# Kernel tuning notes

Measured on AMD Instinct MI355X. Metric: run time of the kernel, lower is better.

The kernel has to match this reference:

```python
import jax, jax.numpy as jnp
import numpy as np

B, T = 64, 500
N_EX, N_SK = 10000, 100
H, K = 128, 32


def setup_inputs() -> dict:
    key = jax.random.key(0)
    ks = jax.random.split(key, 32)
    g = lambda i, shape, s=0.05: (jax.random.normal(ks[i], shape, dtype=jnp.float32) * s)
    inp = {
        's_data': jax.random.randint(ks[0], (B, T), 0, N_SK),
        'a_data': jax.random.randint(ks[1], (B, T), 0, 2),
        'e_data': jax.random.randint(ks[2], (B, T), 0, N_EX),
        'at_data': jax.random.randint(ks[3], (B, T), 0, 100),
        'q_matrix': (jax.random.uniform(ks[4], (N_EX + 1, N_SK + 1)) < 0.05).astype(jnp.float32),
        's_embed_w': g(5, (N_SK + 1, H)),
        'a_embed_w': g(6, (2, H)),
        'e_embed_w': g(7, (N_EX + 1, H)),
        'W1': g(8, (H, 2 * H)), 'b1': jnp.zeros((H,), jnp.float32),
        'W2': g(9, (H, 3 * H)), 'b2': jnp.zeros((H,), jnp.float32),
        'W3': g(10, (H, 2 * H)), 'b3': jnp.zeros((H,), jnp.float32),
        'key_matrix': g(11, (K, H)),
        'gru_w_ih': g(12, (3 * H, H)), 'gru_w_hh': g(13, (3 * H, H)),
        'gru_b_ih': jnp.zeros((3 * H,), jnp.float32), 'gru_b_hh': jnp.zeros((3 * H,), jnp.float32),
        'Wg': g(14, (H, 2 * H)), 'bg': jnp.zeros((H,), jnp.float32),
        'Wgg': g(15, (H, 2 * H)), 'bgg': jnp.zeros((H,), jnp.float32),
        'Wf': g(16, (H, 2 * H)), 'bf': jnp.zeros((H,), jnp.float32),
        'Wp': g(17, (1, 3 * H)), 'bp': jnp.zeros((1,), jnp.float32),
        'Wp1': g(18, (1, 3 * H)), 'bp1': jnp.zeros((1,), jnp.float32),
        'h0': g(19, (H,)),           # xavier init of GRU initial state (shared across batch)
        'm0': g(20, (K, H)),         # xavier init of memory h_pre (shared across batch)
    }
    return inp


def reference(s_data, a_data, e_data, at_data, q_matrix, s_embed_w, a_embed_w, e_embed_w,
              W1, b1, W2, b2, W3, b3, key_matrix, gru_w_ih, gru_w_hh, gru_b_ih, gru_b_hh,
              Wg, bg, Wgg, bgg, Wf, bf, Wp, bp, Wp1, bp1, h0, m0):
    # eval mode: dropout = identity
    Bv, Tv = a_data.shape
    lin = lambda x, W, b: x @ W.T + b
    # ---- embedding (n_exercise > 0 branch) ----
    rel = q_matrix[e_data]                              # [B,T,S+1]
    ssum = rel.sum(-1, keepdims=True)
    ssum = jnp.where(ssum == 0, 1.0, ssum)
    s_emb = jnp.einsum('bts,sh->bth', rel, s_embed_w) / ssum
    e_emb = e_embed_w[e_data]
    a_emb = a_embed_w[a_data]
    se_data = jax.nn.relu(lin(jnp.concatenate([s_emb, e_emb], -1), W1, b1))
    se_learning = jax.nn.relu(lin(jnp.concatenate([s_emb, e_emb, a_emb], -1), W2, b2))
    e_learning = jax.nn.relu(lin(jnp.concatenate([e_emb, a_emb], -1), W3, b3))
    # ---- GRU over e_learning ----
    gx = jnp.einsum('bth,gh->btg', e_learning, gru_w_ih) + gru_b_ih  # [B,T,3H]
    def gru_step(h, gxt):
        gh = h @ gru_w_hh.T + gru_b_hh
        xr, xz, xn = jnp.split(gxt, 3, -1)
        hr, hz, hn = jnp.split(gh, 3, -1)
        r = jax.nn.sigmoid(xr + hr)
        z = jax.nn.sigmoid(xz + hz)
        n = jnp.tanh(xn + r * hn)
        hn2 = (1 - z) * n + z * h
        return hn2, hn2
    _, gru_out = jax.lax.scan(gru_step, jnp.broadcast_to(h0, (Bv, h0.shape[0])), jnp.swapaxes(gx, 0, 1))
    out = jnp.swapaxes(gru_out, 0, 1)[:, :-1]           # [B,T-1,H]
    # ---- key-value memory scan ----
    Wall = jnp.einsum('bth,kh->btk', se_data, key_matrix)  # attention weights (unnormalized)
    h_pre0 = jnp.broadcast_to(m0, (Bv,) + m0.shape)        # [B,K,H]
    ht0 = jnp.einsum('bk,bkh->bh', Wall[:, 0], h_pre0)
    xs = (jnp.swapaxes(Wall[:, :-1], 0, 1),
          jnp.swapaxes(Wall[:, 1:], 0, 1),
          jnp.swapaxes(se_learning[:, :-1], 0, 1))
    def step(carry, x):
        h_pre, ht_pre = carry
        w, w_next, learning = x
        hl = jnp.concatenate([ht_pre, learning], -1)
        gain = jnp.tanh(hl @ Wg.T + bg)
        gate = jax.nn.sigmoid(hl @ Wgg.T + bgg)
        LG = gate * gain                                  # [B,H]
        LG_t = w[:, :, None] * LG[:, None, :]             # [B,K,H] write
        gam = jax.nn.sigmoid(jnp.concatenate([h_pre, jnp.broadcast_to(LG[:, None, :], h_pre.shape)], -1) @ Wf.T + bf)
        h = gam * h_pre + LG_t
        ht = jnp.einsum('bk,bkh->bh', w_next, h)          # read at t+1
        return (h, ht), ht
    _, hts = jax.lax.scan(step, (h_pre0, ht0), xs)
    out1 = jnp.swapaxes(hts, 0, 1)                        # [B,T-1,H]
    sg = jax.lax.stop_gradient
    res = jax.nn.sigmoid(jnp.concatenate([out, sg(out1), e_emb[:, 1:]], -1) @ Wp.T + bp)[..., 0]
    res1 = jax.nn.sigmoid(jnp.concatenate([sg(out), out1, se_data[:, 1:]], -1) @ Wp1.T + bp1)[..., 0]
    pred = jnp.zeros((Bv, Tv), res.dtype).at[:, 1:].set(res * res1)
    return pred
```

## Files before the change

### kernel.cpp

```cpp
#include <hip/hip_runtime.h>

#define TT 500
typedef __attribute__((ext_vector_type(8))) short short8v;
typedef __attribute__((ext_vector_type(4))) short short4v;
typedef __attribute__((ext_vector_type(4))) float float4v;
typedef unsigned short ushort;

__device__ __forceinline__ ushort f2bf(float f) {
  union { float f; unsigned u; } v; v.f = f;
  unsigned r = v.u + 0x7FFFu + ((v.u >> 16) & 1u);
  return (ushort)(r >> 16);
}
__device__ __forceinline__ float bf2f(ushort u) {
  union { unsigned u; float f; } v; v.u = ((unsigned)u) << 16;
  return v.f;
}
__device__ __forceinline__ float sigm(float x) {
  return __builtin_amdgcn_rcpf(1.f + __builtin_amdgcn_exp2f(-1.44269504088896341f * x));
}
__device__ __forceinline__ float tanh_f(float x) {
  return 1.f - 2.f * __builtin_amdgcn_rcpf(1.f + __builtin_amdgcn_exp2f(2.88539008177792682f * x));
}
__device__ __forceinline__ void bar_lds() {
  asm volatile("s_waitcnt lgkmcnt(0)\ns_barrier" ::: "memory");
}
template <int CTRL>
__device__ __forceinline__ float dppadd(float v) {
  int a = __builtin_amdgcn_update_dpp(0, __builtin_bit_cast(int, v), CTRL, 0xF, 0xF, true);
  return v + __builtin_bit_cast(float, a);
}
__device__ __forceinline__ float rsum16(float v) {
  v = dppadd<0xB1>(v);
  v = dppadd<0x4E>(v);
  v = dppadd<0x141>(v);
  v = dppadd<0x140>(v);
  return v;
}
#define MFMA __builtin_amdgcn_mfma_f32_16x16x32_bf16

__global__ __launch_bounds__(256) void conv_k(
    const float* __restrict__ W1, const float* __restrict__ W2,
    const float* __restrict__ W3, const float* __restrict__ Wih,
    const float* __restrict__ key, const float* __restrict__ Wg,
    const float* __restrict__ Wgg, ushort* __restrict__ wts)
{
  int idx = blockIdx.x * 256 + threadIdx.x;
  if (idx >= 200704) return;
  float v;
  if (idx < 32768)       v = W1[idx];
  else if (idx < 81920)  v = W2[idx - 32768];
  else if (idx < 114688) v = W3[idx - 81920];
  else if (idx < 163840) v = Wih[idx - 114688];
  else if (idx < 167936) v = key[idx - 163840];
  else {
    int j = idx - 167936, o = j >> 7, k = j & 127;
    v = (o < 128) ? Wg[o * 256 + 128 + k] : Wgg[(o - 128) * 256 + 128 + k];
  }
  wts[idx] = f2bf(v);
}

#define XS 424
#define SS 648

__global__ __launch_bounds__(256, 2) void phase1_k(
    const int* __restrict__ a_data, const int* __restrict__ e_data,
    const float* __restrict__ qm, const float* __restrict__ semb,
    const float* __restrict__ aemb, const float* __restrict__ eemb,
    const float* __restrict__ b1, const float* __restrict__ b2,
    const float* __restrict__ b3, const float* __restrict__ bih,
    const float* __restrict__ bg, const float* __restrict__ bgg,
    const float* __restrict__ Wp, const float* __restrict__ bp,
    const float* __restrict__ Wp1, const float* __restrict__ bp1,
    const ushort* __restrict__ wts,
    ushort* __restrict__ gxb, ushort* __restrict__ xgx,
    float* __restrict__ wallb, float* __restrict__ c1b, float* __restrict__ c2b)
{
  __shared__ __align__(16) ushort sbuf[27136];
  ushort* Xl = sbuf;
  ushort* Yl = sbuf + 13568;
  ushort* St = sbuf;
  const int tid = threadIdx.x;
  const int b = blockIdx.x >> 4, chunk = blockIdx.x & 15;
  const int t0 = chunk * 32;
  const int NT = (TT - t0 < 32) ? (TT - t0) : 32;
  const ushort* w1b  = wts;
  const ushort* w2b  = wts + 32768;
  const ushort* w3b  = wts + 81920;
  const ushort* wihb = wts + 114688;
  const ushort* keyb = wts + 163840;
  const ushort* wgb  = wts + 167936;

#pragma unroll
  for (int pass = 0; pass < 2; ++pass) {
    const int tok = (tid >> 4) + pass * 16, l16 = tid & 15;
    const int tsrc = (tok < NT) ? tok : (NT - 1);
    const int gt = b * TT + t0 + tsrc;
    const int e = e_data[gt], a = a_data[gt];
    const float* qrow = qm + (size_t)e * 101;
    float qv[7];
#pragma unroll
    for (int i = 0; i < 7; ++i) {
      int s = l16 + 16 * i;
      qv[i] = (s < 101) ? qrow[s] : 0.f;
    }
    const float* sbase = semb + l16 * 8;
    float4v acc0 = {0,0,0,0}, acc1 = {0,0,0,0};
    float cnt = 0.f;
#pragma unroll
    for (int i = 0; i < 7; ++i) {
      unsigned long long bal = __ballot(qv[i] != 0.f);
      unsigned m = (unsigned)((bal >> (tid & 48)) & 0xFFFFull);
      cnt += (float)__popc(m);
      while (m) {
        int s = 16 * i + __builtin_ctz(m);
        m &= m - 1;
        acc0 += *(const float4v*)(sbase + s * 128);
        acc1 += *(const float4v*)(sbase + s * 128 + 4);
      }
    }
    float inv = 1.f / fmaxf(cnt, 1.f);
    ushort* xr = Xl + tok * XS + l16 * 8;
#pragma unroll
    for (int r = 0; r < 4; ++r) { xr[r] = f2bf(acc0[r] * inv); xr[4 + r] = f2bf(acc1[r] * inv); }
    const float* ee = eemb + (size_t)e * 128 + l16 * 8;
    const float* ae = aemb + a * 128 + l16 * 8;
    ushort* xe = Xl + tok * XS + 128 + l16 * 8;
    ushort* xa = Xl + tok * XS + 256 + l16 * 8;
#pragma unroll
    for (int r = 0; r < 8; ++r) { xe[r] = f2bf(ee[r]); xa[r] = f2bf(ae[r]); }
  }
  __syncthreads();

  const int w = tid >> 6, l = tid & 63, jj = l & 15, seg = l >> 4;

  if (tid < 32) {
    int tau = tid;
    if (tau < NT) {
      const ushort* xr = Xl + tau * XS + 128;
      const float* wv = Wp + 256;
      float a0 = bp[0], a1 = 0.f, a2 = 0.f, a3 = 0.f;
      for (int j = 0; j < 128; j += 4) {
        a0 = fmaf(wv[j],     bf2f(xr[j]),     a0);
        a1 = fmaf(wv[j + 1], bf2f(xr[j + 1]), a1);
        a2 = fmaf(wv[j + 2], bf2f(xr[j + 2]), a2);
        a3 = fmaf(wv[j + 3], bf2f(xr[j + 3]), a3);
      }
      c1b[b * TT + t0 + tau] = (a0 + a1) + (a2 + a3);
    }
  }

  short8v axA[12], axB[12];
#pragma unroll
  for (int i = 0; i < 12; ++i) {
    axA[i] = *(short8v*)(Xl + jj * XS + i * 32 + seg * 8);
    axB[i] = *(short8v*)(Xl + (16 + jj) * XS + i * 32 + seg * 8);
  }

  for (int T = w; T < 24; T += 4) {
    float4v dA = {0,0,0,0}, dB = {0,0,0,0};
    float bv;
    if (T < 8) {
      const ushort* Bp = w1b + (T * 16 + jj) * 256 + seg * 8;
      bv = b1[T * 16 + jj];
#pragma unroll
      for (int k = 0; k < 8; ++k) {
        short8v bw = *(const short8v*)(Bp + k * 32);
        dA = MFMA(axA[k], bw, dA, 0, 0, 0);
        dB = MFMA(axB[k], bw, dB, 0, 0, 0);
      }
    } else if (T < 16) {
      const ushort* Bp = w2b + ((T - 8) * 16 + jj) * 384 + seg * 8;
      bv = b2[(T - 8) * 16 + jj];
#pragma unroll
      for (int k = 0; k < 12; ++k) {
        short8v bw = *(const short8v*)(Bp + k * 32);
        dA = MFMA(axA[k], bw, dA, 0, 0, 0);
        dB = MFMA(axB[k], bw, dB, 0, 0, 0);
      }
    } else {
      const ushort* Bp = w3b + ((T - 16) * 16 + jj) * 256 + seg * 8;
      bv = b3[(T - 16) * 16 + jj];
#pragma unroll
      for (int k = 0; k < 8; ++k) {
        short8v bw = *(const short8v*)(Bp + k * 32);
        dA = MFMA(axA[4 + k], bw, dA, 0, 0, 0);
        dB = MFMA(axB[4 + k], bw, dB, 0, 0, 0);
      }
    }
#pragma unroll
    for (int r = 0; r < 4; ++r) {
      float yA = dA[r] + bv, yB = dB[r] + bv;
      Yl[(seg * 4 + r) * XS + T * 16 + jj]        = f2bf(yA > 0.f ? yA : 0.f);
      Yl[(16 + seg * 4 + r) * XS + T * 16 + jj]   = f2bf(yB > 0.f ? yB : 0.f);
    }
  }
  __syncthreads();

  short8v ayA[12], ayB[12];
#pragma unroll
  for (int i = 0; i < 12; ++i) {
    ayA[i] = *(short8v*)(Yl + jj * XS + i * 32 + seg * 8);
    ayB[i] = *(short8v*)(Yl + (16 + jj) * XS + i * 32 + seg * 8);
  }

  if (tid >= 32 && tid < 64) {
    int tau = tid - 32;
    if (tau < NT) {
      const ushort* xr = Yl + tau * XS;
      const float* wv = Wp1 + 256;
      float a0 = bp1[0], a1 = 0.f, a2 = 0.f, a3 = 0.f;
      for (int j = 0; j < 128; j += 4) {
        a0 = fmaf(wv[j],     bf2f(xr[j]),     a0);
        a1 = fmaf(wv[j + 1], bf2f(xr[j + 1]), a1);
        a2 = fmaf(wv[j + 2], bf2f(xr[j + 2]), a2);
        a3 = fmaf(wv[j + 3], bf2f(xr[j + 3]), a3);
      }
      c2b[b * TT + t0 + tau] = (a0 + a1) + (a2 + a3);
    }
  }
  __syncthreads();

  for (int T = w; T < 42; T += 4) {
    const ushort* Bp; int ai;
    if (T < 24)      { Bp = wihb + (T * 16 + jj) * 128 + seg * 8;        ai = 8; }
    else if (T < 40) { Bp = wgb  + ((T - 24) * 16 + jj) * 128 + seg * 8; ai = 4; }
    else             { Bp = keyb + ((T - 40) * 16 + jj) * 128 + seg * 8; ai = 0; }
    float4v dA = {0,0,0,0}, dB = {0,0,0,0};
#pragma unroll
    for (int k = 0; k < 4; ++k) {
      short8v bw = *(const short8v*)(Bp + k * 32);
      dA = MFMA(ayA[ai + k], bw, dA, 0, 0, 0);
      dB = MFMA(ayB[ai + k], bw, dB, 0, 0, 0);
    }
    if (T < 40) {
      float bv = (T < 24) ? bih[T * 16 + jj]
               : (T < 32) ? bg[(T - 24) * 16 + jj] : bgg[(T - 32) * 16 + jj];
      int col = (T < 24) ? (T * 16 + jj) : (384 + (T - 24) * 16 + jj);
#pragma unroll
      for (int r = 0; r < 4; ++r) {
        St[(seg * 4 + r) * SS + col]      = f2bf(dA[r] + bv);
        St[(16 + seg * 4 + r) * SS + col] = f2bf(dB[r] + bv);
      }
    } else {
#pragma unroll
      for (int r = 0; r < 4; ++r) {
        int tokA = seg * 4 + r, tokB = 16 + seg * 4 + r;
        if (tokA < NT)
          wallb[((size_t)(b * TT + t0 + tokA)) * 32 + (T - 40) * 16 + jj] = dA[r];
        if (tokB < NT)
          wallb[((size_t)(b * TT + t0 + tokB)) * 32 + (T - 40) * 16 + jj] = dB[r];
      }
    }
  }
  __syncthreads();

#pragma unroll
  for (int pass = 0; pass < 2; ++pass) {
    const int tok = (tid >> 4) + pass * 16, sg = tid & 15;
    if (tok < NT) {
      size_t gt = (size_t)b * TT + t0 + tok;
#pragma unroll
      for (int p = 0; p < 3; ++p)
        *(short8v*)(gxb + gt * 384 + sg * 24 + p * 8) = *(short8v*)(St + tok * SS + sg * 24 + p * 8);
#pragma unroll
      for (int p = 0; p < 2; ++p)
        *(short8v*)(xgx + gt * 256 + sg * 16 + p * 8) = *(short8v*)(St + tok * SS + 384 + sg * 16 + p * 8);
    }
  }
}

__global__ __launch_bounds__(512) void scan_k(
    const float* __restrict__ Wf, const float* __restrict__ bf_,
    const float* __restrict__ Wg, const float* __restrict__ Wgg,
    const float* __restrict__ Whh, const float* __restrict__ bhh,
    const float* __restrict__ h0v, const float* __restrict__ m0,
    const ushort* __restrict__ gxb, const ushort* __restrict__ xgx,
    const float* __restrict__ wallb,
    ushort* __restrict__ htsm, ushort* __restrict__ htsg)
{
  const int tid = threadIdx.x;
  const int w = tid >> 6, l = tid & 63, jj = l & 15, seg = l >> 4;
  const int n0 = w * 16 + seg * 4;

  if (blockIdx.x < 64) {
    const int b = blockIdx.x;
    __shared__ __align__(16) ushort h_bf[32 * 128];
    __shared__ __align__(16) ushort htb[128];
    __shared__ __align__(16) ushort LGb[128];

    short8v afrA[4], aggA[4], aggB[4], alg[4];
#pragma unroll
    for (int ks = 0; ks < 4; ++ks) {
      const float* sA = Wf  + (w * 16 + jj) * 256 + ks * 32 + seg * 8;
      const float* sB = Wg  + (w * 16 + jj) * 256 + ks * 32 + seg * 8;
      const float* sC = Wgg + (w * 16 + jj) * 256 + ks * 32 + seg * 8;
      const float* sD = Wf  + (w * 16 + jj) * 256 + 128 + ks * 32 + seg * 8;
      short8v a, bb, c, d;
#pragma unroll
      for (int j = 0; j < 8; ++j) {
        a[j] = (short)f2bf(sA[j]); bb[j] = (short)f2bf(sB[j]);
        c[j] = (short)f2bf(sC[j]); d[j] = (short)f2bf(sD[j]);
      }
      afrA[ks] = a; aggA[ks] = bb; aggB[ks] = c; alg[ks] = d;
    }
    const float4v bf4 = *(const float4v*)(bf_ + n0);

    float hreg[2][4];
#pragma unroll
    for (int nt = 0; nt < 2; ++nt) {
      int k = nt * 16 + jj;
      float4v m = *(const float4v*)(m0 + k * 128 + n0);
#pragma unroll
      for (int r = 0; r < 4; ++r) hreg[nt][r] = m[r];
      int p = ((n0 >> 3) + k) & 15;
      short4v pk;
#pragma unroll
      for (int r = 0; r < 4; ++r) pk[r] = (short)f2bf(hreg[nt][r]);
      *(short4v*)(h_bf + k * 128 + p * 8 + (n0 & 7)) = pk;
    }
    const float* wl = wallb + (size_t)b * TT * 32;
    const ushort* xgp = xgx + (size_t)b * TT * 256;
    float wv0 = wl[jj], wv1 = wl[16 + jj];
    float wn0 = wl[32 + jj], wn1 = wl[48 + jj];
    short4v xcg  = *(const short4v*)(xgp + n0);
    short4v xcgg = *(const short4v*)(xgp + 128 + n0);
    short4v xng  = *(const short4v*)(xgp + 256 + n0);
    short4v xngg = *(const short4v*)(xgp + 384 + n0);
    {
      float4v htp;
#pragma unroll
      for (int r = 0; r < 4; ++r)
        htp[r] = rsum16(wv0 * hreg[0][r] + wv1 * hreg[1][r]);
      if (jj == 0) {
        short4v hp;
#pragma unroll
        for (int r = 0; r < 4; ++r) hp[r] = (short)f2bf(htp[r]);
        *(short4v*)(htb + n0) = hp;
      }
    }
    __syncthreads();

    for (int t = 0; t < TT - 1; ++t) {
      int tw = (t + 2 <= TT - 1) ? (t + 2) : (TT - 1);
      float wf0 = wl[tw * 32 + jj], wf1 = wl[tw * 32 + 16 + jj];
      short4v xfg  = *(const short4v*)(xgp + (size_t)tw * 256 + n0);
      short4v xfgg = *(const short4v*)(xgp + (size_t)tw * 256 + 128 + n0);

      short8v hb[4];
#pragma unroll
      for (int ks = 0; ks < 4; ++ks)
        hb[ks] = *(short8v*)(htb + ks * 32 + seg * 8);
      short8v bv0[4], bv1[4];
#pragma unroll
      for (int ks = 0; ks < 4; ++ks) {
        int g = ks * 4 + seg;
        bv0[ks] = *(short8v*)(h_bf + jj * 128 + ((g + jj) & 15) * 8);
        bv1[ks] = *(short8v*)(h_bf + (16 + jj) * 128 + ((g + 16 + jj) & 15) * 8);
      }

      float4v xg4, xgg4;
#pragma unroll
      for (int r = 0; r < 4; ++r) { xg4[r] = bf2f((ushort)xcg[r]); xgg4[r] = bf2f((ushort)xcgg[r]); }
      float4v dg0 = xg4, dg1 = {0,0,0,0}, gg0 = xgg4, gg1 = {0,0,0,0};
      dg0 = MFMA(aggA[0], hb[0], dg0, 0, 0, 0);
      dg0 = MFMA(aggA[1], hb[1], dg0, 0, 0, 0);
      dg1 = MFMA(aggA[2], hb[2], dg1, 0, 0, 0);
      dg1 = MFMA(aggA[3], hb[3], dg1, 0, 0, 0);
      gg0 = MFMA(aggB[0], hb[0], gg0, 0, 0, 0);
      gg0 = MFMA(aggB[1], hb[1], gg0, 0, 0, 0);
      gg1 = MFMA(aggB[2], hb[2], gg1, 0, 0, 0);
      gg1 = MFMA(aggB[3], hb[3], gg1, 0, 0, 0);

      float4v a0A = {0,0,0,0}, a0B = {0,0,0,0}, a1A = {0,0,0,0}, a1B = {0,0,0,0};
      a0A = MFMA(afrA[0], bv0[0], a0A, 0, 0, 0);
      a0A = MFMA(afrA[1], bv0[1], a0A, 0, 0, 0);
      a0B = MFMA(afrA[2], bv0[2], a0B, 0, 0, 0);
      a0B = MFMA(afrA[3], bv0[3], a0B, 0, 0, 0);
      a1A = MFMA(afrA[0], bv1[0], a1A, 0, 0, 0);
      a1A = MFMA(afrA[1], bv1[1], a1A, 0, 0, 0);
      a1B = MFMA(afrA[2], bv1[2], a1B, 0, 0, 0);
      a1B = MFMA(afrA[3], bv1[3], a1B, 0, 0, 0);

      float lgv[4];
#pragma unroll
      for (int r = 0; r < 4; ++r)
        lgv[r] = tanh_f(dg0[r] + dg1[r]) * sigm(gg0[r] + gg1[r]);
      if (jj == 0) {
        short4v lp;
#pragma unroll
        for (int r = 0; r < 4; ++r) lp[r] = (short)f2bf(lgv[r]);
        *(short4v*)(LGb + n0) = lp;
      }
      bar_lds();

      short8v lb[4];
#pragma unroll
      for (int ks = 0; ks < 4; ++ks)
        lb[ks] = *(short8v*)(LGb + ks * 32 + seg * 8);
      float4v dl0 = bf4, dl1 = {0,0,0,0};
      dl0 = MFMA(alg[0], lb[0], dl0, 0, 0, 0);
      dl0 = MFMA(alg[1], lb[1], dl0, 0, 0, 0);
      dl1 = MFMA(alg[2], lb[2], dl1, 0, 0, 0);
      dl1 = MFMA(alg[3], lb[3], dl1, 0, 0, 0);

      float4v htp = {0,0,0,0};
#pragma unroll
      for (int nt = 0; nt < 2; ++nt) {
        float wvv = nt ? wv1 : wv0;
        float wnn = nt ? wn1 : wn0;
#pragma unroll
        for (int r = 0; r < 4; ++r) {
          float a = nt ? (a1A[r] + a1B[r]) : (a0A[r] + a0B[r]);
          float gam = sigm(a + dl0[r] + dl1[r]);
          float hn = fmaf(gam, hreg[nt][r], wvv * lgv[r]);
          hreg[nt][r] = hn;
          htp[r] = fmaf(wnn, hn, htp[r]);
        }
        int k = nt * 16 + jj;
        int p = ((n0 >> 3) + k) & 15;
        short4v pk;
#pragma unroll
        for (int r = 0; r < 4; ++r) pk[r] = (short)f2bf(hreg[nt][r]);
        *(short4v*)(h_bf + k * 128 + p * 8 + (n0 & 7)) = pk;
      }
#pragma unroll
      for (int r = 0; r < 4; ++r) htp[r] = rsum16(htp[r]);
      if (jj == 0) {
        short4v hp;
#pragma unroll
        for (int r = 0; r < 4; ++r) hp[r] = (short)f2bf(htp[r]);
        *(short4v*)(htb + n0) = hp;
        *(short4v*)(htsm + ((size_t)b * TT + t) * 128 + n0) = hp;
      }
      wv0 = wn0; wv1 = wn1; wn0 = wf0; wn1 = wf1;
      xcg = xng; xcgg = xngg; xng = xfg; xngg = xfgg;
      bar_lds();
    }
  } else {
    const int b = blockIdx.x - 64;
    __shared__ __align__(16) ushort hb2[2][128];

    short8v wfr[3][4];
    float4v bfr[3];
#pragma unroll
    for (int i = 0; i < 3; ++i) {
      int Mt = w + i * 8;
#pragma unroll
      for (int ks = 0; ks < 4; ++ks) {
        const float* src = Whh + (Mt * 16 + jj) * 128 + ks * 32 + seg * 8;
        short8v tv;
#pragma unroll
        for (int j = 0; j < 8; ++j) tv[j] = (short)f2bf(src[j]);
        wfr[i][ks] = tv;
      }
      bfr[i] = *(const float4v*)(bhh + Mt * 16 + seg * 4);
    }
    const ushort* gpb = gxb + (size_t)b * TT * 384;
    float4v hj4 = *(const float4v*)(h0v + n0);
    if (jj == 0) {
      short4v hp;
#pragma unroll
      for (int r = 0; r < 4; ++r) hp[r] = (short)f2bf(hj4[r]);
      *(short4v*)(&hb2[0][n0]) = hp;
    }
    short4v xr_c = *(const short4v*)(gpb + n0);
    short4v xz_c = *(const short4v*)(gpb + 128 + n0);
    short4v xn_c = *(const short4v*)(gpb + 256 + n0);
    short4v xr_n = *(const short4v*)(gpb + 384 + n0);
    short4v xz_n = *(const short4v*)(gpb + 512 + n0);
    short4v xn_n = *(const short4v*)(gpb + 640 + n0);
    __syncthreads();

    for (int t = 0; t < TT - 1; ++t) {
      int tf = (t + 2 < TT - 1) ? (t + 2) : (TT - 2);
      const ushort* gf = gpb + (size_t)tf * 384;
      short4v xr_f = *(const short4v*)(gf + n0);
      short4v xz_f = *(const short4v*)(gf + 128 + n0);
      short4v xn_f = *(const short4v*)(gf + 256 + n0);

      const ushort* hsrc = hb2[t & 1];
      short8v bfrg[4];
#pragma unroll
      for (int ks = 0; ks < 4; ++ks)
        bfrg[ks] = *(short8v*)(hsrc + ks * 32 + seg * 8);

      float4v a0A = bfr[0], a1A = bfr[1], a2A = bfr[2];
      float4v a0B = {0,0,0,0}, a1B = {0,0,0,0}, a2B = {0,0,0,0};
      a0A = MFMA(wfr[0][0], bfrg[0], a0A, 0, 0, 0);
      a0A = MFMA(wfr[0][1], bfrg[1], a0A, 0, 0, 0);
      a0B = MFMA(wfr[0][2], bfrg[2], a0B, 0, 0, 0);
      a0B = MFMA(wfr[0][3], bfrg[3], a0B, 0, 0, 0);
      a1A = MFMA(wfr[1][0], bfrg[0], a1A, 0, 0, 0);
      a1A = MFMA(wfr[1][1], bfrg[1], a1A, 0, 0, 0);
      a1B = MFMA(wfr[1][2], bfrg[2], a1B, 0, 0, 0);
      a1B = MFMA(wfr[1][3], bfrg[3], a1B, 0, 0, 0);
      a2A = MFMA(wfr[2][0], bfrg[0], a2A, 0, 0, 0);
      a2A = MFMA(wfr[2][1], bfrg[1], a2A, 0, 0, 0);
      a2B = MFMA(wfr[2][2], bfrg[2], a2B, 0, 0, 0);
      a2B = MFMA(wfr[2][3], bfrg[3], a2B, 0, 0, 0);

      ushort* hdst = (ushort*)hb2[(t + 1) & 1];
      short4v hp;
#pragma unroll
      for (int r = 0; r < 4; ++r) {
        float rr = sigm(bf2f((ushort)xr_c[r]) + a0A[r] + a0B[r]);
        float zz = sigm(bf2f((ushort)xz_c[r]) + a1A[r] + a1B[r]);
        float nn = tanh_f(bf2f((ushort)xn_c[r]) + rr * (a2A[r] + a2B[r]));
        hj4[r] = fmaf(1.f - zz, nn, zz * hj4[r]);
        hp[r] = (short)f2bf(hj4[r]);
      }
      if (jj == 0) {
        *(short4v*)(hdst + n0) = hp;
        *(short4v*)(htsg + ((size_t)b * TT + t) * 128 + n0) = hp;
      }
      xr_c = xr_n; xz_c = xz_n; xn_c = xn_n;
      xr_n = xr_f; xz_n = xz_f; xn_n = xn_f;
      bar_lds();
    }
  }
}

__global__ __launch_bounds__(256) void combine_k(
    const ushort* __restrict__ htsg, const ushort* __restrict__ htsm,
    const float* __restrict__ c1b, const float* __restrict__ c2b,
    const float* __restrict__ Wp, const float* __restrict__ Wp1,
    float* __restrict__ out)
{
  const int b = blockIdx.x;
  const int wv = threadIdx.x >> 6;
  const int lane = threadIdx.x & 63;
  const float w0 = Wp[lane], w1 = Wp[64 + lane], w2 = Wp[128 + lane], w3 = Wp[192 + lane];
  const float v0 = Wp1[lane], v1 = Wp1[64 + lane], v2 = Wp1[128 + lane], v3 = Wp1[192 + lane];
  if (threadIdx.x == 0) out[(size_t)b * TT] = 0.f;
  for (int tau = wv; tau < TT - 1; tau += 4) {
    size_t base = ((size_t)b * TT + tau) * 128;
    float hg0 = bf2f(htsg[base + lane]), hg1 = bf2f(htsg[base + 64 + lane]);
    float hm0 = bf2f(htsm[base + lane]), hm1 = bf2f(htsm[base + 64 + lane]);
    float qa = hg0 * w0 + hg1 * w1 + hm0 * w2 + hm1 * w3;
    float qb = hg0 * v0 + hg1 * v1 + hm0 * v2 + hm1 * v3;
#pragma unroll
    for (int m = 1; m < 64; m <<= 1) {
      qa += __shfl_xor(qa, m, 64);
      qb += __shfl_xor(qb, m, 64);
    }
    if (lane == 0) {
      size_t idx = (size_t)b * TT + tau + 1;
      out[idx] = sigm(qa + c1b[idx]) * sigm(qb + c2b[idx]);
    }
  }
}

extern "C" void kernel_launch(void* const* d_in, const int* in_sizes, int n_in,
                              void* d_out, int out_size, void* d_ws, size_t ws_size,
                              hipStream_t stream) {
  (void)in_sizes; (void)n_in; (void)out_size; (void)ws_size;
  const int* a_data = (const int*)d_in[1];
  const int* e_data = (const int*)d_in[2];
  const float* qm   = (const float*)d_in[4];
  const float* semb = (const float*)d_in[5];
  const float* aemb = (const float*)d_in[6];
  const float* eemb = (const float*)d_in[7];
  const float* W1 = (const float*)d_in[8];   const float* b1 = (const float*)d_in[9];
  const float* W2 = (const float*)d_in[10];  const float* b2 = (const float*)d_in[11];
  const float* W3 = (const float*)d_in[12];  const float* b3 = (const float*)d_in[13];
  const float* key = (const float*)d_in[14];
  const float* Wih = (const float*)d_in[15]; const float* Whh = (const float*)d_in[16];
  const float* bih = (const float*)d_in[17]; const float* bhh = (const float*)d_in[18];
  const float* Wg  = (const float*)d_in[19]; const float* bg  = (const float*)d_in[20];
  const float* Wgg = (const float*)d_in[21]; const float* bgg = (const float*)d_in[22];
  const float* Wf  = (const float*)d_in[23]; const float* bf_ = (const float*)d_in[24];
  const float* Wp  = (const float*)d_in[25]; const float* bp  = (const float*)d_in[26];
  const float* Wp1 = (const float*)d_in[27]; const float* bp1 = (const float*)d_in[28];
  const float* h0v = (const float*)d_in[29]; const float* m0  = (const float*)d_in[30];

  char* ws = (char*)d_ws;
  ushort* gxb  = (ushort*)(ws + 0);
  ushort* xgx  = (ushort*)(ws + 24576000);
  float* wallb = (float*)(ws + 40960000);
  ushort* htsm = (ushort*)(ws + 45056000);
  ushort* htsg = (ushort*)(ws + 53248000);
  float* c1b   = (float*)(ws + 61440000);
  float* c2b   = (float*)(ws + 61568000);
  ushort* wts  = (ushort*)(ws + 61696000);
  float* out = (float*)d_out;

  conv_k<<<dim3(784), dim3(256), 0, stream>>>(W1, W2, W3, Wih, key, Wg, Wgg, wts);
  phase1_k<<<dim3(1024), dim3(256), 0, stream>>>(
      a_data, e_data, qm, semb, aemb, eemb, b1, b2, b3, bih, bg, bgg,
      Wp, bp, Wp1, bp1, wts, gxb, xgx, wallb, c1b, c2b);
  scan_k<<<dim3(128), dim3(512), 0, stream>>>(
      Wf, bf_, Wg, Wgg, Whh, bhh, h0v, m0, gxb, xgx, wallb, htsm, htsg);
  combine_k<<<dim3(64), dim3(256), 0, stream>>>(
      htsg, htsm, c1b, c2b, Wp, Wp1, out);
}
```

Before: 954.0 us.

## Split embedding gather into own kernel, reorder scan LG write, cheaper bf16 rounding

Moves the q-matrix/embedding gather out of the GEMM kernel into a separate fully-parallel kernel that writes bf16 rows to a workspace buffer (gxb), which the GEMM kernel then loads with vector copies. In the memory scan, the gain/gate computation and LG store are moved ahead of the h_bf loads and MFMAs, so they are off the critical path before the barrier. A cheaper round-half-up bf16 conversion replaces round-to-nearest-even in the scan loops. The split adds a kernel launch and a global round trip, and reuses gxb, which the GEMM also writes as output, so there may be an aliasing conflict.

```diff
diff --git a/kernel.cpp b/kernel.cpp
--- a/kernel.cpp
+++ b/kernel.cpp
@@ -10,6 +10,10 @@
   union { float f; unsigned u; } v; v.f = f;
   unsigned r = v.u + 0x7FFFu + ((v.u >> 16) & 1u);
   return (ushort)(r >> 16);
+}
+__device__ __forceinline__ ushort f2bfr(float f) {
+  union { float f; unsigned u; } v; v.f = f;
+  return (ushort)((v.u + 0x8000u) >> 16);
 }
 __device__ __forceinline__ float bf2f(ushort u) {
   union { unsigned u; float f; } v; v.u = ((unsigned)u) << 16;
@@ -59,13 +63,55 @@
   wts[idx] = f2bf(v);
 }
 
-#define XS 424
-#define SS 648
-
-__global__ __launch_bounds__(256, 2) void phase1_k(
+__global__ __launch_bounds__(256) void ph_gather_k(
     const int* __restrict__ a_data, const int* __restrict__ e_data,
     const float* __restrict__ qm, const float* __restrict__ semb,
     const float* __restrict__ aemb, const float* __restrict__ eemb,
+    ushort* __restrict__ Xg)
+{
+  const int tid = threadIdx.x;
+  const int tok = tid >> 4, l16 = tid & 15;
+  const int gt = blockIdx.x * 16 + tok;
+  const int e = e_data[gt], a = a_data[gt];
+  const float* qrow = qm + (size_t)e * 101;
+  float qv[7];
+#pragma unroll
+  for (int i = 0; i < 7; ++i) {
+    int s = l16 + 16 * i;
+    qv[i] = (s < 101) ? qrow[s] : 0.f;
+  }
+  const float* sbase = semb + l16 * 8;
+  float4v acc0 = {0,0,0,0}, acc1 = {0,0,0,0};
+  float cnt = 0.f;
+#pragma unroll
+  for (int i = 0; i < 7; ++i) {
+    unsigned long long bal = __ballot(qv[i] != 0.f);
+    unsigned m = (unsigned)((bal >> (tid & 48)) & 0xFFFFull);
+    cnt += (float)__popc(m);
+    while (m) {
+      int s = 16 * i + __builtin_ctz(m);
+      m &= m - 1;
+      acc0 += *(const float4v*)(sbase + s * 128);
+      acc1 += *(const float4v*)(sbase + s * 128 + 4);
+    }
+  }
+  float inv = 1.f / fmaxf(cnt, 1.f);
+  ushort* xr = Xg + (size_t)gt * 384 + l16 * 8;
+  const float* ee = eemb + (size_t)e * 128 + l16 * 8;
+  const float* ae = aemb + a * 128 + l16 * 8;
+  short4v p0, p1;
+#pragma unroll
+  for (int r = 0; r < 4; ++r) { p0[r] = (short)f2bf(acc0[r] * inv); p1[r] = (short)f2bf(acc1[r] * inv); }
+  *(short4v*)(xr) = p0;
+  *(short4v*)(xr + 4) = p1;
+#pragma unroll
+  for (int r = 0; r < 8; ++r) { xr[128 + r] = f2bf(ee[r]); xr[256 + r] = f2bf(ae[r]); }
+}
+
+#define XS 424
+#define SS 648
+
+__global__ __launch_bounds__(256, 2) void ph_gemm_k(
     const float* __restrict__ b1, const float* __restrict__ b2,
     const float* __restrict__ b3, const float* __restrict__ bih,
     const float* __restrict__ bg, const float* __restrict__ bgg,
@@ -92,42 +138,12 @@
 
 #pragma unroll
   for (int pass = 0; pass < 2; ++pass) {
-    const int tok = (tid >> 4) + pass * 16, l16 = tid & 15;
+    const int tok = (tid >> 4) + pass * 16, sg = tid & 15;
     const int tsrc = (tok < NT) ? tok : (NT - 1);
-    const int gt = b * TT + t0 + tsrc;
-    const int e = e_data[gt], a = a_data[gt];
-    const float* qrow = qm + (size_t)e * 101;
-    float qv[7];
-#pragma unroll
-    for (int i = 0; i < 7; ++i) {
-      int s = l16 + 16 * i;
-      qv[i] = (s < 101) ? qrow[s] : 0.f;
-    }
-    const float* sbase = semb + l16 * 8;
-    float4v acc0 = {0,0,0,0}, acc1 = {0,0,0,0};
-    float cnt = 0.f;
-#pragma unroll
-    for (int i = 0; i < 7; ++i) {
-      unsigned long long bal = __ballot(qv[i] != 0.f);
-      unsigned m = (unsigned)((bal >> (tid & 48)) & 0xFFFFull);
-      cnt += (float)__popc(m);
-      while (m) {
-        int s = 16 * i + __builtin_ctz(m);
-        m &= m - 1;
-        acc0 += *(const float4v*)(sbase + s * 128);
-        acc1 += *(const float4v*)(sbase + s * 128 + 4);
-      }
-    }
-    float inv = 1.f / fmaxf(cnt, 1.f);
-    ushort* xr = Xl + tok * XS + l16 * 8;
-#pragma unroll
-    for (int r = 0; r < 4; ++r) { xr[r] = f2bf(acc0[r] * inv); xr[4 + r] = f2bf(acc1[r] * inv); }
-    const float* ee = eemb + (size_t)e * 128 + l16 * 8;
-    const float* ae = aemb + a * 128 + l16 * 8;
-    ushort* xe = Xl + tok * XS + 128 + l16 * 8;
-    ushort* xa = Xl + tok * XS + 256 + l16 * 8;
-#pragma unroll
-    for (int r = 0; r < 8; ++r) { xe[r] = f2bf(ee[r]); xa[r] = f2bf(ae[r]); }
+    size_t gt = (size_t)b * TT + t0 + tsrc;
+#pragma unroll
+    for (int p = 0; p < 3; ++p)
+      *(short8v*)(Xl + tok * XS + sg * 24 + p * 8) = *(const short8v*)(gxb + gt * 384 + sg * 24 + p * 8);
   }
   __syncthreads();
 
@@ -190,8 +206,8 @@
 #pragma unroll
     for (int r = 0; r < 4; ++r) {
       float yA = dA[r] + bv, yB = dB[r] + bv;
-      Yl[(seg * 4 + r) * XS + T * 16 + jj]        = f2bf(yA > 0.f ? yA : 0.f);
-      Yl[(16 + seg * 4 + r) * XS + T * 16 + jj]   = f2bf(yB > 0.f ? yB : 0.f);
+      Yl[(seg * 4 + r) * XS + T * 16 + jj]      = f2bf(yA > 0.f ? yA : 0.f);
+      Yl[(16 + seg * 4 + r) * XS + T * 16 + jj] = f2bf(yB > 0.f ? yB : 0.f);
     }
   }
   __syncthreads();
@@ -350,13 +366,6 @@
 #pragma unroll
       for (int ks = 0; ks < 4; ++ks)
         hb[ks] = *(short8v*)(htb + ks * 32 + seg * 8);
-      short8v bv0[4], bv1[4];
-#pragma unroll
-      for (int ks = 0; ks < 4; ++ks) {
-        int g = ks * 4 + seg;
-        bv0[ks] = *(short8v*)(h_bf + jj * 128 + ((g + jj) & 15) * 8);
-        bv1[ks] = *(short8v*)(h_bf + (16 + jj) * 128 + ((g + 16 + jj) & 15) * 8);
-      }
 
       float4v xg4, xgg4;
 #pragma unroll
@@ -371,6 +380,24 @@
       gg1 = MFMA(aggB[2], hb[2], gg1, 0, 0, 0);
       gg1 = MFMA(aggB[3], hb[3], gg1, 0, 0, 0);
 
+      float lgv[4];
+#pragma unroll
+      for (int r = 0; r < 4; ++r)
+        lgv[r] = tanh_f(dg0[r] + dg1[r]) * sigm(gg0[r] + gg1[r]);
+      if (jj == 0) {
+        short4v lp;
+#pragma unroll
+        for (int r = 0; r < 4; ++r) lp[r] = (short)f2bfr(lgv[r]);
+        *(short4v*)(LGb + n0) = lp;
+      }
+
+      short8v bv0[4], bv1[4];
+#pragma unroll
+      for (int ks = 0; ks < 4; ++ks) {
+        int g = ks * 4 + seg;
+        bv0[ks] = *(short8v*)(h_bf + jj * 128 + ((g + jj) & 15) * 8);
+        bv1[ks] = *(short8v*)(h_bf + (16 + jj) * 128 + ((g + 16 + jj) & 15) * 8);
+      }
       float4v a0A = {0,0,0,0}, a0B = {0,0,0,0}, a1A = {0,0,0,0}, a1B = {0,0,0,0};
       a0A = MFMA(afrA[0], bv0[0], a0A, 0, 0, 0);
       a0A = MFMA(afrA[1], bv0[1], a0A, 0, 0, 0);
@@ -380,17 +407,6 @@
       a1A = MFMA(afrA[1], bv1[1], a1A, 0, 0, 0);
       a1B = MFMA(afrA[2], bv1[2], a1B, 0, 0, 0);
       a1B = MFMA(afrA[3], bv1[3], a1B, 0, 0, 0);
-
-      float lgv[4];
-#pragma unroll
-      for (int r = 0; r < 4; ++r)
-        lgv[r] = tanh_f(dg0[r] + dg1[r]) * sigm(gg0[r] + gg1[r]);
-      if (jj == 0) {
-        short4v lp;
-#pragma unroll
-        for (int r = 0; r < 4; ++r) lp[r] = (short)f2bf(lgv[r]);
-        *(short4v*)(LGb + n0) = lp;
-      }
       bar_lds();
 
       short8v lb[4];
@@ -420,7 +436,7 @@
         int p = ((n0 >> 3) + k) & 15;
         short4v pk;
 #pragma unroll
-        for (int r = 0; r < 4; ++r) pk[r] = (short)f2bf(hreg[nt][r]);
+        for (int r = 0; r < 4; ++r) pk[r] = (short)f2bfr(hreg[nt][r]);
         *(short4v*)(h_bf + k * 128 + p * 8 + (n0 & 7)) = pk;
       }
 #pragma unroll
@@ -428,7 +444,7 @@
       if (jj == 0) {
         short4v hp;
 #pragma unroll
-        for (int r = 0; r < 4; ++r) hp[r] = (short)f2bf(htp[r]);
+        for (int r = 0; r < 4; ++r) hp[r] = (short)f2bfr(htp[r]);
         *(short4v*)(htb + n0) = hp;
         *(short4v*)(htsm + ((size_t)b * TT + t) * 128 + n0) = hp;
       }
@@ -507,7 +523,7 @@
         float zz = sigm(bf2f((ushort)xz_c[r]) + a1A[r] + a1B[r]);
         float nn = tanh_f(bf2f((ushort)xn_c[r]) + rr * (a2A[r] + a2B[r]));
         hj4[r] = fmaf(1.f - zz, nn, zz * hj4[r]);
-        hp[r] = (short)f2bf(hj4[r]);
+        hp[r] = (short)f2bfr(hj4[r]);
       }
       if (jj == 0) {
         *(short4v*)(hdst + n0) = hp;
@@ -585,9 +601,11 @@
   float* out = (float*)d_out;
 
   conv_k<<<dim3(784), dim3(256), 0, stream>>>(W1, W2, W3, Wih, key, Wg, Wgg, wts);
-  phase1_k<<<dim3(1024), dim3(256), 0, stream>>>(
-      a_data, e_data, qm, semb, aemb, eemb, b1, b2, b3, bih, bg, bgg,
-      Wp, bp, Wp1, bp1, wts, gxb, xgx, wallb, c1b, c2b);
+  ph_gather_k<<<dim3(2000), dim3(256), 0, stream>>>(
+      a_data, e_data, qm, semb, aemb, eemb, gxb);
+  ph_gemm_k<<<dim3(1024), dim3(256), 0, stream>>>(
+      b1, b2, b3, bih, bg, bgg, Wp, bp, Wp1, bp1, wts,
+      gxb, xgx, wallb, c1b, c2b);
   scan_k<<<dim3(128), dim3(512), 0, stream>>>(
       Wf, bf_, Wg, Wgg, Whh, bhh, h0v, m0, gxb, xgx, wallb, htsm, htsg);
   combine_k<<<dim3(64), dim3(256), 0, stream>>>(
```

Result: no change. 949.9 us (-0.4%).
